# Optimization experiments

Measured on AMD Instinct MI355X. Metric: run time of the kernel, lower is better.

Reference implementation:

```python
import jax, jax.numpy as jnp
import numpy as np

NUM_HEADS = 16
HIDDEN = 1024
HEAD_DIM = HIDDEN // NUM_HEADS
B, L = 2, 2048


def setup_inputs() -> dict:
    key = jax.random.key(0)
    ks = jax.random.split(key, 5)
    scale = 1.0 / np.sqrt(HIDDEN)
    return {
        "x": jax.random.normal(ks[0], (B, L, HIDDEN), dtype=jnp.float32),
        "Wq": jax.random.normal(ks[1], (HIDDEN, HIDDEN), dtype=jnp.float32) * scale,
        "Wk": jax.random.normal(ks[2], (HIDDEN, HIDDEN), dtype=jnp.float32) * scale,
        "Wv": jax.random.normal(ks[3], (HIDDEN, HIDDEN), dtype=jnp.float32) * scale,
        "Wo": jax.random.normal(ks[4], (HIDDEN, HIDDEN), dtype=jnp.float32) * scale,
    }


def reference(x, Wq, Wk, Wv, Wo):
    b, l, _ = x.shape
    # projections (torch nn.Linear: y = x @ W.T), reshape to (B,L,H,D)
    q = (x @ Wq.T).reshape(b, l, NUM_HEADS, HEAD_DIM)
    k = (x @ Wk.T).reshape(b, l, NUM_HEADS, HEAD_DIM)
    v = (x @ Wv.T).reshape(b, l, NUM_HEADS, HEAD_DIM)
    # positive feature map
    q = jax.nn.elu(q) + 1.0
    k = jax.nn.elu(k) + 1.0
    # causal linear attention via cumulative kv outer products
    kv = jnp.einsum('blhd,blhe->blhde', k, v)          # (B,L,H,D,D)
    kv_cumsum = jnp.cumsum(kv, axis=1)
    k_cumsum = jnp.cumsum(k, axis=1)
    out = jnp.einsum('blhd,blhde->blhe', q, kv_cumsum)  # (B,L,H,D)
    normalizer = jnp.clip(jnp.einsum('blhd,blhd->blh', q, k_cumsum), 1e-6, None)
    out = out / normalizer[..., None]
    out = out.reshape(b, l, HIDDEN)
    return out @ Wo.T
```

## Files before the change

### kernel.cpp

```cpp
#include <hip/hip_runtime.h>
#include <cstdint>
#include <cstddef>

#define HID 1024
#define NH 16
#define HD 64
#define BB 2
#define LL 2048
#define MM (BB*LL)
#define CHUNK 64
#define NSEG 16
#define BHn (BB*NH)
#define SP 72

typedef __bf16 bf16;
typedef __attribute__((ext_vector_type(8))) __bf16 bf16x8;
typedef __attribute__((ext_vector_type(4))) float f32x4;

__device__ __forceinline__ f32x4 mfma16(bf16x8 a, bf16x8 b, f32x4 c){
  return __builtin_amdgcn_mfma_f32_16x16x32_bf16(a, b, c, 0, 0, 0);
}

__device__ __forceinline__ void gload16(const void* g, void* l){
  __builtin_amdgcn_global_load_lds(
      (const __attribute__((address_space(1))) unsigned int*)g,
      (__attribute__((address_space(3))) unsigned int*)l, 16, 0, 0);
}

__device__ __forceinline__ void barx(){
  asm volatile("" ::: "memory");
  __builtin_amdgcn_s_barrier();
  asm volatile("" ::: "memory");
}

#define WAITVM(N) asm volatile("s_waitcnt vmcnt(" #N ")" ::: "memory")

__global__ __launch_bounds__(256) void cast_all_k(
    const float* __restrict__ x,  const float* __restrict__ w0,
    const float* __restrict__ w1, const float* __restrict__ w2, const float* __restrict__ w3,
    bf16* __restrict__ xb, bf16* __restrict__ d0, bf16* __restrict__ d1,
    bf16* __restrict__ d2, bf16* __restrict__ d3)
{
  int bid = blockIdx.x;
  const float* s; bf16* d; int base;
  if (bid < 2048){ s = x; d = xb; base = bid; }
  else {
    int w = (bid - 2048) >> 9, r = (bid - 2048) & 511;
    s = (w==0)?w0:(w==1)?w1:(w==2)?w2:w3;
    d = (w==0)?d0:(w==1)?d1:(w==2)?d2:d3;
    base = r;
  }
  size_t i = (size_t)(base*256 + threadIdx.x) * 8;
  float4 v0 = *(const float4*)(s + i);
  float4 v1 = *(const float4*)(s + i + 4);
  union { bf16 h[8]; uint4 u; } pk;
  pk.h[0]=(bf16)v0.x; pk.h[1]=(bf16)v0.y; pk.h[2]=(bf16)v0.z; pk.h[3]=(bf16)v0.w;
  pk.h[4]=(bf16)v1.x; pk.h[5]=(bf16)v1.y; pk.h[6]=(bf16)v1.z; pk.h[7]=(bf16)v1.w;
  *(uint4*)(d + i) = pk.u;
}

template<int MODE>
__global__ __launch_bounds__(512, 2) void gemm8_k(
    const bf16* __restrict__ A,
    const bf16* __restrict__ W0, const bf16* __restrict__ W1, const bf16* __restrict__ W2,
    bf16* __restrict__ Qo, bf16* __restrict__ Kn, bf16* __restrict__ Vn,
    float* __restrict__ Outf)
{
  constexpr int NKT = HID/32;
  __shared__ bf16 lds[3][2][128*32];

  const int tid = threadIdx.x;
  const int wv = tid >> 6, lane = tid & 63;
  const int lrow = lane & 15, g4 = lane >> 4;
  const int wr = wv >> 2, wc = wv & 3;
  int bn = blockIdx.x, wsel = 0;
  const bf16* W = W0;
  if (MODE==0){ wsel = bn >> 3; bn &= 7; W = (wsel==0)?W0:((wsel==1)?W1:W2); }
  const int row0 = blockIdx.y*128, col0 = bn*128;

  const int sr = tid >> 2, sc = tid & 3;
  const int scs = sc ^ ((sr>>1)&3);
  const bf16* gA = A + (size_t)(row0 + sr)*HID + scs*8;
  const bf16* gB = W + (size_t)(col0 + sr)*HID + scs*8;
  const int ldst = tid*8;

  auto stage_tile = [&](int u){
    const int buf = u % 3;
    gload16(gA + u*32, (void*)&lds[buf][0][ldst]);
    gload16(gB + u*32, (void*)&lds[buf][1][ldst]);
  };

  const int koff = (g4 ^ ((lrow>>1)&3)) << 3;

  auto read_frags = [&](int u, bf16x8 (&fa)[4], bf16x8 (&fb)[2]){
    const int buf = u % 3;
    #pragma unroll
    for (int i=0;i<4;i++)
      fa[i] = *(const bf16x8*)&lds[buf][0][((wr*64 + i*16+lrow)<<5) + koff];
    #pragma unroll
    for (int j=0;j<2;j++)
      fb[j] = *(const bf16x8*)&lds[buf][1][((wc*32 + j*16+lrow)<<5) + koff];
  };

  f32x4 acc[4][2] = {};
  auto do_mfma = [&](bf16x8 (&fa)[4], bf16x8 (&fb)[2]){
    __builtin_amdgcn_s_setprio(1);
    #pragma unroll
    for (int i=0;i<4;i++)
      #pragma unroll
      for (int j=0;j<2;j++)
        acc[i][j] = mfma16(fa[i], fb[j], acc[i][j]);
    __builtin_amdgcn_s_setprio(0);
  };

  stage_tile(0); stage_tile(1);
  WAITVM(2);
  barx();
  bf16x8 fEa[4], fEb[2], fOa[4], fOb[2];
  read_frags(0, fEa, fEb);

  for (int t=0; t<NKT; t+=2){
    if (t+2 < NKT){ stage_tile(t+2); WAITVM(2); }
    else          { WAITVM(0); }
    barx();
    read_frags(t+1, fOa, fOb);
    do_mfma(fEa, fEb);
    const int t2 = t+1;
    if (t2 < NKT-1){
      if (t2+2 < NKT){ stage_tile(t2+2); WAITVM(2); }
      else           { WAITVM(0); }
      barx();
      read_frags(t2+1, fEa, fEb);
    }
    do_mfma(fOa, fOb);
  }

  #pragma unroll
  for (int i=0;i<4;i++){
    const int m0 = row0 + wr*64 + i*16 + g4*4;
    #pragma unroll
    for (int j=0;j<2;j++){
      const int c = col0 + wc*32 + j*16 + lrow;
      #pragma unroll
      for (int r=0;r<4;r++){
        float v = acc[i][j][r];
        if (MODE==1){
          Outf[(size_t)(m0+r)*HID + c] = v;
        } else {
          if (wsel<2) v = v>0.f ? v+1.f : __expf(v);
          bf16 bv = (bf16)v;
          if      (wsel==0) Qo[(size_t)(m0+r)*HID + c] = bv;
          else if (wsel==1) Kn[(size_t)(m0+r)*HID + c] = bv;
          else              Vn[(size_t)(m0+r)*HID + c] = bv;
        }
      }
    }
  }
}

__global__ __launch_bounds__(256, 2) void segsum_k(const bf16* __restrict__ Kn, const bf16* __restrict__ Vn,
                                                   float* __restrict__ Sseg, float* __restrict__ kseg)
{
  __shared__ bf16 KT[64*SP];
  __shared__ bf16 VT[64*SP];
  const int bx = blockIdx.x;
  const int bh = bx >> 4, seg = bx & (NSEG-1);
  const int b = bh>>4, h = bh&15;
  const int tid = threadIdx.x;
  const int we = tid >> 6, lane = tid & 63;
  const int lrow = lane&15, g4 = lane>>4, lk8 = g4*8;
  const int sj = tid >> 2, c4 = tid & 3;

  f32x4 acc[4] = {};
  float krow = 0.f;

  #pragma unroll
  for (int c=0;c<2;c++){
    const int cg = seg*2 + c;
    const bf16* kb = Kn + ((size_t)(b*LL + cg*CHUNK))*HID + h*HD;
    const bf16* vb = Vn + ((size_t)(b*LL + cg*CHUNK))*HID + h*HD;
    {
      const bf16* ks = kb + (size_t)sj*HID + c4*16;
      const bf16* vs = vb + (size_t)sj*HID + c4*16;
      bf16x8 kr0 = *(const bf16x8*)&ks[0], kr1 = *(const bf16x8*)&ks[8];
      bf16x8 vr0 = *(const bf16x8*)&vs[0], vr1 = *(const bf16x8*)&vs[8];
      #pragma unroll
      for (int e=0;e<8;e++){
        KT[(c4*16+e)*SP + sj]   = kr0[e];
        KT[(c4*16+8+e)*SP + sj] = kr1[e];
        VT[(c4*16+e)*SP + sj]   = vr0[e];
        VT[(c4*16+8+e)*SP + sj] = vr1[e];
      }
    }
    __syncthreads();
    #pragma unroll
    for (int kk=0;kk<2;kk++){
      bf16x8 fa = *(const bf16x8*)&VT[(we*16 + lrow)*SP + kk*32 + lk8];
      #pragma unroll
      for (int j=0;j<4;j++){
        bf16x8 fb = *(const bf16x8*)&KT[(j*16 + lrow)*SP + kk*32 + lk8];
        acc[j] = mfma16(fa, fb, acc[j]);
      }
    }
    {
      const int row = we*16 + lrow;
      float s = 0.f;
      #pragma unroll
      for (int u=0;u<2;u++){
        bf16x8 k8 = *(const bf16x8*)&KT[row*SP + g4*16 + u*8];
        #pragma unroll
        for (int e=0;e<8;e++) s += (float)k8[e];
      }
      s += __shfl_xor(s,16); s += __shfl_xor(s,32);
      krow += s;
    }
    __syncthreads();
  }

  float* so = Sseg + (size_t)bx*4096;
  #pragma unroll
  for (int j=0;j<4;j++)
    #pragma unroll
    for (int r=0;r<4;r++)
      so[(we*16 + g4*4 + r)*64 + j*16 + lrow] = acc[j][r];
  if (g4==0) kseg[(size_t)bx*64 + we*16 + lrow] = krow;
}

__global__ __launch_bounds__(256) void segscan_k(const float* __restrict__ Sseg, const float* __restrict__ kseg,
                                                 bf16* __restrict__ Sexb, float* __restrict__ ksxb)
{
  int gid = blockIdx.x*256 + threadIdx.x;
  if (gid < BHn*4096){
    int bh = gid >> 12, e = gid & 4095;
    float run = 0.f;
    size_t base = (size_t)bh*NSEG*4096 + e;
    #pragma unroll 4
    for (int s=0;s<NSEG;s++){
      Sexb[base + (size_t)s*4096] = (bf16)run;
      run += Sseg[base + (size_t)s*4096];
    }
  } else if (gid < BHn*4096 + BHn*64){
    int g2 = gid - BHn*4096;
    int bh = g2 >> 6, d = g2 & 63;
    float run = 0.f;
    size_t base = (size_t)bh*NSEG*64 + d;
    #pragma unroll 4
    for (int s=0;s<NSEG;s++){
      ksxb[base + (size_t)s*64] = run;
      run += kseg[base + (size_t)s*64];
    }
  }
}

__global__ __launch_bounds__(256, 2) void attn_k(const bf16* __restrict__ Q, const bf16* __restrict__ Kn,
                                                 const bf16* __restrict__ Vn, const bf16* __restrict__ Sexb,
                                                 const float* __restrict__ ksxb, bf16* __restrict__ Obuf)
{
  __shared__ bf16 KT[64*SP];
  __shared__ bf16 VT[64*SP];
  __shared__ bf16 P [64*SP];
  __shared__ bf16 Sm[64*SP];
  __shared__ float ksum_lds[64];
  const int bx = blockIdx.x;
  const int bh = bx >> 4, seg = bx & (NSEG-1);
  const int b = bh>>4, h = bh&15;
  const int tid = threadIdx.x;
  const int w = tid >> 6, lane = tid & 63;
  const int lrow = lane&15, g4 = lane>>4, lk8 = g4*8;
  const int sj = tid >> 2, c4 = tid & 3;

  if (tid < 64) ksum_lds[tid] = ksxb[(size_t)bx*64 + tid];
  {
    const bf16* sp = Sexb + (size_t)bx*4096 + tid*16;
    bf16x8 s0 = *(const bf16x8*)&sp[0], s1 = *(const bf16x8*)&sp[8];
    const int e = tid>>2, d0 = (tid&3)*16;
    *(bf16x8*)&Sm[e*SP + d0]     = s0;
    *(bf16x8*)&Sm[e*SP + d0 + 8] = s1;
  }
  __syncthreads();
  f32x4 Srun[4];
  #pragma unroll
  for (int j=0;j<4;j++)
    #pragma unroll
    for (int r=0;r<4;r++)
      Srun[j][r] = (float)Sm[(w*16+g4*4+r)*SP + j*16+lrow];

  #pragma unroll
  for (int c=0;c<2;c++){
    const int cg = seg*2 + c;
    const bf16* kb = Kn + ((size_t)(b*LL + cg*CHUNK))*HID + h*HD;
    const bf16* vb = Vn + ((size_t)(b*LL + cg*CHUNK))*HID + h*HD;
    const bf16* qb = Q  + ((size_t)(b*LL + cg*CHUNK))*HID + h*HD;
    {
      const bf16* ks = kb + (size_t)sj*HID + c4*16;
      const bf16* vs = vb + (size_t)sj*HID + c4*16;
      bf16x8 kr0 = *(const bf16x8*)&ks[0], kr1 = *(const bf16x8*)&ks[8];
      bf16x8 vr0 = *(const bf16x8*)&vs[0], vr1 = *(const bf16x8*)&vs[8];
      #pragma unroll
      for (int e=0;e<8;e++){
        KT[(c4*16+e)*SP + sj]   = kr0[e];
        KT[(c4*16+8+e)*SP + sj] = kr1[e];
        VT[(c4*16+e)*SP + sj]   = vr0[e];
        VT[(c4*16+8+e)*SP + sj] = vr1[e];
      }
    }
    bf16x8 aq[2], bk[4][2];
    #pragma unroll
    for (int kk=0;kk<2;kk++){
      aq[kk] = *(const bf16x8*)&qb[(size_t)(w*16+lrow)*HID + kk*32 + lk8];
      #pragma unroll
      for (int j=0;j<4;j++)
        bk[j][kk] = *(const bf16x8*)&kb[(size_t)(j*16+lrow)*HID + kk*32 + lk8];
    }
    __syncthreads();
    f32x4 sacc[4] = {};
    #pragma unroll
    for (int kk=0;kk<2;kk++)
      #pragma unroll
      for (int j=0;j<4;j++)
        sacc[j] = mfma16(aq[kk], bk[j][kk], sacc[j]);
    float rs[4];
    #pragma unroll
    for (int r=0;r<4;r++){
      int irow = w*16 + g4*4 + r;
      float p = 0.f;
      #pragma unroll
      for (int j=0;j<4;j++){
        int jcol = j*16 + lrow;
        float v = (jcol <= irow) ? sacc[j][r] : 0.f;
        sacc[j][r] = v;
        p += v;
      }
      p += __shfl_xor(p,1); p += __shfl_xor(p,2);
      p += __shfl_xor(p,4); p += __shfl_xor(p,8);
      rs[r] = p;
    }
    float zA;
    {
      float s = 0.f;
      #pragma unroll
      for (int kk=0;kk<2;kk++){
        const float* k8 = ksum_lds + kk*32 + lk8;
        bf16x8 q = aq[kk];
        #pragma unroll
        for (int j=0;j<8;j++) s += (float)q[j] * k8[j];
      }
      s += __shfl_xor(s,16); s += __shfl_xor(s,32);
      zA = s;
    }
    f32x4 oacc[4] = {};
    #pragma unroll
    for (int kk=0;kk<2;kk++)
      #pragma unroll
      for (int j=0;j<4;j++){
        bf16x8 bs = *(const bf16x8*)&Sm[(j*16+lrow)*SP + kk*32 + lk8];
        oacc[j] = mfma16(aq[kk], bs, oacc[j]);
      }
    #pragma unroll
    for (int j=0;j<4;j++)
      #pragma unroll
      for (int r=0;r<4;r++)
        P[(w*16+g4*4+r)*SP + j*16+lrow] = (bf16)sacc[j][r];
    __syncthreads();
    #pragma unroll
    for (int kk=0;kk<2;kk++){
      bf16x8 ap = *(const bf16x8*)&P[(w*16+lrow)*SP + kk*32 + lk8];
      #pragma unroll
      for (int j=0;j<4;j++){
        bf16x8 bv = *(const bf16x8*)&VT[(j*16+lrow)*SP + kk*32 + lk8];
        oacc[j] = mfma16(ap, bv, oacc[j]);
      }
    }
    bf16* ob = Obuf + ((size_t)(b*LL + cg*CHUNK))*HID + h*HD;
    #pragma unroll
    for (int r=0;r<4;r++){
      float z = __shfl(zA, g4*4 + r) + rs[r];
      z = fmaxf(z, 1e-6f);
      float inv = 1.0f/z;
      int irow = w*16 + g4*4 + r;
      #pragma unroll
      for (int j=0;j<4;j++)
        ob[(size_t)irow*HID + j*16+lrow] = (bf16)(oacc[j][r]*inv);
    }
    if (c==0){
      #pragma unroll
      for (int kk=0;kk<2;kk++){
        bf16x8 fa = *(const bf16x8*)&VT[(w*16+lrow)*SP + kk*32 + lk8];
        #pragma unroll
        for (int j=0;j<4;j++){
          bf16x8 fb = *(const bf16x8*)&KT[(j*16+lrow)*SP + kk*32 + lk8];
          Srun[j] = mfma16(fa, fb, Srun[j]);
        }
      }
      {
        const int row = w*16 + lrow;
        float s = 0.f;
        #pragma unroll
        for (int u=0;u<2;u++){
          bf16x8 k8 = *(const bf16x8*)&KT[row*SP + g4*16 + u*8];
          #pragma unroll
          for (int e=0;e<8;e++) s += (float)k8[e];
        }
        s += __shfl_xor(s,16); s += __shfl_xor(s,32);
        if (g4==0) ksum_lds[row] += s;
      }
      #pragma unroll
      for (int j=0;j<4;j++)
        #pragma unroll
        for (int r=0;r<4;r++)
          Sm[(w*16+g4*4+r)*SP + j*16+lrow] = (bf16)Srun[j][r];
    }
    __syncthreads();
  }
}

extern "C" void kernel_launch(void* const* d_in, const int* in_sizes, int n_in,
                              void* d_out, int out_size, void* d_ws, size_t ws_size,
                              hipStream_t stream)
{
  const float* x  = (const float*)d_in[0];
  const float* Wq = (const float*)d_in[1];
  const float* Wk = (const float*)d_in[2];
  const float* Wv = (const float*)d_in[3];
  const float* Wo = (const float*)d_in[4];
  float* out = (float*)d_out;

  char* p = (char*)d_ws;
  auto alloc = [&](size_t bytes){ void* r = (void*)p; p += (bytes + 255) & ~(size_t)255; return r; };
  bf16* xb   = (bf16*)alloc((size_t)MM*HID*2);
  bf16* Wqb  = (bf16*)alloc((size_t)HID*HID*2);
  bf16* Wkb  = (bf16*)alloc((size_t)HID*HID*2);
  bf16* Wvb  = (bf16*)alloc((size_t)HID*HID*2);
  bf16* Wob  = (bf16*)alloc((size_t)HID*HID*2);
  bf16* Qb   = (bf16*)alloc((size_t)MM*HID*2);
  bf16* Knb  = (bf16*)alloc((size_t)MM*HID*2);
  bf16* Vnb  = (bf16*)alloc((size_t)MM*HID*2);
  bf16* Ob   = (bf16*)alloc((size_t)MM*HID*2);
  float* Sseg = (float*)alloc((size_t)BHn*NSEG*4096*4);
  bf16*  Sexb = (bf16*) alloc((size_t)BHn*NSEG*4096*2);
  float* kseg = (float*)alloc((size_t)BHn*NSEG*64*4);
  float* ksxb = (float*)alloc((size_t)BHn*NSEG*64*4);

  cast_all_k<<<dim3(4096), 256, 0, stream>>>(x, Wq,Wk,Wv,Wo, xb, Wqb,Wkb,Wvb,Wob);
  gemm8_k<0><<<dim3(24,32), 512, 0, stream>>>(xb, Wqb,Wkb,Wvb, Qb,Knb,Vnb, nullptr);
  segsum_k<<<dim3(BHn*NSEG), 256, 0, stream>>>(Knb, Vnb, Sseg, kseg);
  segscan_k<<<dim3((BHn*4096 + BHn*64 + 255)/256), 256, 0, stream>>>(Sseg, kseg, Sexb, ksxb);
  attn_k<<<dim3(BHn*NSEG), 256, 0, stream>>>(Qb, Knb, Vnb, Sexb, ksxb, Ob);
  gemm8_k<1><<<dim3(8,32), 512, 0, stream>>>(Ob, Wob,nullptr,nullptr, nullptr,nullptr,nullptr, out);
}
```

Before: 155.8 us.

## Switch GEMM to 4-wave 64x64 warp tiles with double buffering

Replaces the 8-wave, triple-buffered GEMM with a 4-wave kernel where each wave computes a 64x64 tile (4x4 MFMA accumulators), doubling per-wave register reuse of fragments. The pipeline becomes a plain two-buffer loop with __syncthreads instead of explicit vmcnt waits and raw barriers. LDS drops to two buffers, allowing more blocks per CU, but the prefetch depth is shallower, there is a full barrier every k-step, and accumulator register pressure is higher.

```diff
diff --git a/kernel.cpp b/kernel.cpp
--- a/kernel.cpp
+++ b/kernel.cpp
@@ -27,14 +27,6 @@
       (__attribute__((address_space(3))) unsigned int*)l, 16, 0, 0);
 }
 
-__device__ __forceinline__ void barx(){
-  asm volatile("" ::: "memory");
-  __builtin_amdgcn_s_barrier();
-  asm volatile("" ::: "memory");
-}
-
-#define WAITVM(N) asm volatile("s_waitcnt vmcnt(" #N ")" ::: "memory")
-
 __global__ __launch_bounds__(256) void cast_all_k(
     const float* __restrict__ x,  const float* __restrict__ w0,
     const float* __restrict__ w1, const float* __restrict__ w2, const float* __restrict__ w3,
@@ -60,87 +52,70 @@
 }
 
 template<int MODE>
-__global__ __launch_bounds__(512, 2) void gemm8_k(
+__global__ __launch_bounds__(256, 3) void gemm4_k(
     const bf16* __restrict__ A,
     const bf16* __restrict__ W0, const bf16* __restrict__ W1, const bf16* __restrict__ W2,
     bf16* __restrict__ Qo, bf16* __restrict__ Kn, bf16* __restrict__ Vn,
     float* __restrict__ Outf)
 {
   constexpr int NKT = HID/32;
-  __shared__ bf16 lds[3][2][128*32];
+  __shared__ bf16 lds[2][2][128*32];
 
   const int tid = threadIdx.x;
   const int wv = tid >> 6, lane = tid & 63;
   const int lrow = lane & 15, g4 = lane >> 4;
-  const int wr = wv >> 2, wc = wv & 3;
+  const int wr = wv >> 1, wc = wv & 1;
   int bn = blockIdx.x, wsel = 0;
   const bf16* W = W0;
   if (MODE==0){ wsel = bn >> 3; bn &= 7; W = (wsel==0)?W0:((wsel==1)?W1:W2); }
   const int row0 = blockIdx.y*128, col0 = bn*128;
 
-  const int sr = tid >> 2, sc = tid & 3;
-  const int scs = sc ^ ((sr>>1)&3);
-  const bf16* gA = A + (size_t)(row0 + sr)*HID + scs*8;
-  const bf16* gB = W + (size_t)(col0 + sr)*HID + scs*8;
-  const int ldst = tid*8;
-
-  auto stage_tile = [&](int u){
-    const int buf = u % 3;
-    gload16(gA + u*32, (void*)&lds[buf][0][ldst]);
-    gload16(gB + u*32, (void*)&lds[buf][1][ldst]);
+  const int srow = (wv<<5) + (lane>>2);
+  const int scs  = (lane&3) ^ ((srow>>1)&3);
+  const bf16* gA = A + (size_t)(row0 + srow)*HID + scs*8;
+  const bf16* gB = W + (size_t)(col0 + srow)*HID + scs*8;
+
+  auto stage_tile = [&](int u, int buf){
+    #pragma unroll
+    for (int q=0;q<2;q++){
+      gload16(gA + u*32 + (size_t)q*16*HID, (void*)&lds[buf][0][((wv<<5)+(q<<4))*32 + lane*8]);
+      gload16(gB + u*32 + (size_t)q*16*HID, (void*)&lds[buf][1][((wv<<5)+(q<<4))*32 + lane*8]);
+    }
   };
 
   const int koff = (g4 ^ ((lrow>>1)&3)) << 3;
 
-  auto read_frags = [&](int u, bf16x8 (&fa)[4], bf16x8 (&fb)[2]){
-    const int buf = u % 3;
+  f32x4 acc[4][4] = {};
+
+  stage_tile(0, 0);
+  __syncthreads();
+  int buf = 0;
+  for (int t=0; t<NKT; ++t){
+    if (t+1 < NKT) stage_tile(t+1, buf^1);
+    bf16x8 fa[4], fb[4];
     #pragma unroll
     for (int i=0;i<4;i++)
       fa[i] = *(const bf16x8*)&lds[buf][0][((wr*64 + i*16+lrow)<<5) + koff];
     #pragma unroll
-    for (int j=0;j<2;j++)
-      fb[j] = *(const bf16x8*)&lds[buf][1][((wc*32 + j*16+lrow)<<5) + koff];
-  };
-
-  f32x4 acc[4][2] = {};
-  auto do_mfma = [&](bf16x8 (&fa)[4], bf16x8 (&fb)[2]){
+    for (int j=0;j<4;j++)
+      fb[j] = *(const bf16x8*)&lds[buf][1][((wc*64 + j*16+lrow)<<5) + koff];
     __builtin_amdgcn_s_setprio(1);
     #pragma unroll
     for (int i=0;i<4;i++)
       #pragma unroll
-      for (int j=0;j<2;j++)
+      for (int j=0;j<4;j++)
         acc[i][j] = mfma16(fa[i], fb[j], acc[i][j]);
     __builtin_amdgcn_s_setprio(0);
-  };
-
-  stage_tile(0); stage_tile(1);
-  WAITVM(2);
-  barx();
-  bf16x8 fEa[4], fEb[2], fOa[4], fOb[2];
-  read_frags(0, fEa, fEb);
-
-  for (int t=0; t<NKT; t+=2){
-    if (t+2 < NKT){ stage_tile(t+2); WAITVM(2); }
-    else          { WAITVM(0); }
-    barx();
-    read_frags(t+1, fOa, fOb);
-    do_mfma(fEa, fEb);
-    const int t2 = t+1;
-    if (t2 < NKT-1){
-      if (t2+2 < NKT){ stage_tile(t2+2); WAITVM(2); }
-      else           { WAITVM(0); }
-      barx();
-      read_frags(t2+1, fEa, fEb);
-    }
-    do_mfma(fOa, fOb);
+    __syncthreads();
+    buf ^= 1;
   }
 
   #pragma unroll
   for (int i=0;i<4;i++){
     const int m0 = row0 + wr*64 + i*16 + g4*4;
     #pragma unroll
-    for (int j=0;j<2;j++){
-      const int c = col0 + wc*32 + j*16 + lrow;
+    for (int j=0;j<4;j++){
+      const int c = col0 + wc*64 + j*16 + lrow;
       #pragma unroll
       for (int r=0;r<4;r++){
         float v = acc[i][j][r];
@@ -442,9 +417,9 @@
   float* ksxb = (float*)alloc((size_t)BHn*NSEG*64*4);
 
   cast_all_k<<<dim3(4096), 256, 0, stream>>>(x, Wq,Wk,Wv,Wo, xb, Wqb,Wkb,Wvb,Wob);
-  gemm8_k<0><<<dim3(24,32), 512, 0, stream>>>(xb, Wqb,Wkb,Wvb, Qb,Knb,Vnb, nullptr);
+  gemm4_k<0><<<dim3(24,32), 256, 0, stream>>>(xb, Wqb,Wkb,Wvb, Qb,Knb,Vnb, nullptr);
   segsum_k<<<dim3(BHn*NSEG), 256, 0, stream>>>(Knb, Vnb, Sseg, kseg);
   segscan_k<<<dim3((BHn*4096 + BHn*64 + 255)/256), 256, 0, stream>>>(Sseg, kseg, Sexb, ksxb);
   attn_k<<<dim3(BHn*NSEG), 256, 0, stream>>>(Qb, Knb, Vnb, Sexb, ksxb, Ob);
-  gemm8_k<1><<<dim3(8,32), 512, 0, stream>>>(Ob, Wob,nullptr,nullptr, nullptr,nullptr,nullptr, out);
-}
+  gemm4_k<1><<<dim3(8,32), 256, 0, stream>>>(Ob, Wob,nullptr,nullptr, nullptr,nullptr,nullptr, out);
+}
```

New measurement: 156.0 us. About the same (+0.2%).
